# Kernel optimization log

Measured on AMD Instinct MI355X. Metric: run time of the kernel, lower is better.

Reference implementation:

```python
import jax, jax.numpy as jnp
import numpy as np

R, E, A, F, K = 1024, 512, 128, 32, 31  # rnn_dim, embed_dim, attn_dim, n_filters, kernel
B, T = 64, 2048


def setup_inputs() -> dict:
    key = jax.random.key(0)
    ks = jax.random.split(key, 10)
    return {
        "attention_hidden": jax.random.normal(ks[0], (B, R), jnp.float32),
        "memory": jax.random.normal(ks[1], (B, T, E), jnp.float32),
        "attention_weights_cat": jax.random.uniform(ks[2], (B, 2, T), jnp.float32),
        "mask": jax.random.randint(ks[3], (B, T), 0, 2, jnp.int32),
        "W_query": jax.random.normal(ks[4], (R, A), jnp.float32) / np.sqrt(R),
        "W_memory": jax.random.normal(ks[5], (E, A), jnp.float32) / np.sqrt(E),
        "conv_w": jax.random.normal(ks[6], (F, 2, K), jnp.float32) / np.sqrt(2 * K),  # OIH
        "W_loc": jax.random.normal(ks[7], (F, A), jnp.float32) / np.sqrt(F),
        "v_w": jax.random.normal(ks[8], (A,), jnp.float32) / np.sqrt(A),
        "v_b": jax.random.normal(ks[9], (1,), jnp.float32) * 0.0,
    }


def reference(attention_hidden, memory, attention_weights_cat, mask,
              W_query, W_memory, conv_w, W_loc, v_w, v_b):
    # processed query: (B, A)
    pq = attention_hidden @ W_query
    # processed memory: (B, T, A)
    pm = jnp.einsum('bte,ea->bta', memory, W_memory)
    # location features: conv1d over (B, 2, T) with 'same' padding, no bias
    loc = jax.lax.conv_general_dilated(
        attention_weights_cat, conv_w,
        window_strides=(1,), padding=[((K - 1) // 2, (K - 1) // 2)],
        dimension_numbers=('NCH', 'OIH', 'NCH'))  # (B, F, T)
    pl = jnp.einsum('bft,fa->bta', loc, W_loc)  # (B, T, A)
    # energies: v(tanh(pm + pq + pl)) -> (B, T)
    energies = jnp.tanh(pm + pq[:, None, :] + pl) @ v_w + v_b[0]
    alignments = energies + mask.astype(energies.dtype) * -1e25
    attention_weights = jax.nn.softmax(alignments, axis=-1)
    # NOTE: original code (faithfully) uses raw alignments, not softmax weights
    attention_output = jnp.einsum('bt,bte->be', alignments, memory)
    return attention_output, attention_weights
```

## Files before the change

### kernel.cpp

```cpp
#include <hip/hip_runtime.h>

#define Bsz 64
#define Tsz 2048
#define Esz 512
#define Asz 128
#define Rsz 1024
#define KP  576
#define TILE_M 32

typedef __bf16 bf16;
typedef __bf16 bf16x8 __attribute__((ext_vector_type(8)));
typedef __bf16 bf16x4 __attribute__((ext_vector_type(4)));
typedef __bf16 bf16x2 __attribute__((ext_vector_type(2)));
typedef float  f32x4  __attribute__((ext_vector_type(4)));

__global__ __launch_bounds__(256) void prep_kernel(
    const float* __restrict__ Wmem, const float* __restrict__ convw,
    const float* __restrict__ Wloc, const float* __restrict__ ah,
    const float* __restrict__ Wq, bf16* __restrict__ Wext,
    float* __restrict__ pq)
{
  __shared__ f32x4 red[256];
  int blk = blockIdx.x, tid = threadIdx.x;
  if (blk < 128) {
    int a = blk;
    #pragma unroll
    for (int e = tid; e < Esz; e += 256)
      Wext[a*KP + e] = (bf16)Wmem[e*Asz + a];
  } else if (blk < 160) {
    int idx = (blk - 128)*256 + tid;
    int a = idx >> 6, j = idx & 63;
    float u = 0.f;
    if (j < 62) {
      int c  = (j < 31) ? 0 : 1;
      int kk = (j < 31) ? j : j - 31;
      #pragma unroll
      for (int f = 0; f < 32; ++f)
        u += convw[f*62 + c*31 + kk] * Wloc[f*Asz + a];
    }
    Wext[a*KP + Esz + j] = (bf16)u;
  } else {
    int b  = blk - 160;
    int cg = tid & 31;
    int kg = tid >> 5;
    const float* ahb = ah + (size_t)b*Rsz;
    f32x4 s = (f32x4){0.f,0.f,0.f,0.f};
    int r0 = kg*128;
    for (int r = r0; r < r0 + 128; ++r) {
      float av = ahb[r];
      f32x4 wq = *(const f32x4*)&Wq[r*Asz + cg*4];
      s += av * wq;
    }
    red[tid] = s;
    __syncthreads();
    if (tid < 32) {
      f32x4 tot = red[tid];
      #pragma unroll
      for (int g = 1; g < 8; ++g) tot += red[g*32 + tid];
      *(f32x4*)&pq[b*Asz + tid*4] = tot;
    }
  }
}

__global__ __launch_bounds__(256) void attn_main(
    const float* __restrict__ memory, const float* __restrict__ awcat,
    const int* __restrict__ mask, const bf16* __restrict__ Wext,
    const float* __restrict__ pq, const float* __restrict__ vw,
    const float* __restrict__ vb, float* __restrict__ out,
    float* __restrict__ ws_align)
{
  __shared__ bf16  Afull[TILE_M * KP];
  __shared__ float s_pq[Asz];
  __shared__ float s_vw[Asz];
  __shared__ float s_ebuf[TILE_M];
  __shared__ float s_align[TILE_M];

  int tid = threadIdx.x;
  int b  = blockIdx.x >> 6;
  int t0 = (blockIdx.x & 63) << 5;

  const float4* memv = (const float4*)(memory + (size_t)(b*Tsz + t0)*Esz);
  #pragma unroll
  for (int i = tid; i < TILE_M*(Esz/4); i += 256) {
    int r = i >> 7, c4 = i & 127;
    float4 v = memv[r*128 + c4];
    int k = c4 * 4;
    int sw = (k >> 3) ^ (r & 7);
    int base = r*KP + sw*8 + (k & 7);
    bf16x4 p; p[0]=(bf16)v.x; p[1]=(bf16)v.y; p[2]=(bf16)v.z; p[3]=(bf16)v.w;
    *(bf16x4*)&Afull[base] = p;
  }
  const float* aw = awcat + (size_t)b*2*Tsz;
  #pragma unroll
  for (int i = tid; i < TILE_M*64; i += 256) {
    int r = i >> 6, j = i & 63;
    float val = 0.f;
    if (j < 62) {
      int c  = (j < 31) ? 0 : 1;
      int kk = (j < 31) ? j : j - 31;
      int t  = t0 + r + kk - 15;
      if (t >= 0 && t < Tsz) val = aw[c*Tsz + t];
    }
    int k = Esz + j;
    int sw = (k >> 3) ^ (r & 7);
    Afull[r*KP + sw*8 + (k & 7)] = (bf16)val;
  }
  if (tid < Asz) { s_pq[tid] = pq[b*Asz + tid]; s_vw[tid] = vw[tid]; }
  if (tid < TILE_M) s_ebuf[tid] = 0.f;
  __syncthreads();

  int w = tid >> 6, l = tid & 63;
  int quad = l >> 4, lrow = l & 15;

  f32x4 acc[2][2];
  #pragma unroll
  for (int mt = 0; mt < 2; ++mt)
    #pragma unroll
    for (int nt = 0; nt < 2; ++nt)
      acc[mt][nt] = (f32x4){0.f, 0.f, 0.f, 0.f};

  for (int kc = 0; kc < KP/32; ++kc) {
    int kbase = kc*32 + quad*8;
    bf16x8 bfrag[2];
    #pragma unroll
    for (int nt = 0; nt < 2; ++nt) {
      int acol = lrow + 16*(2*w + nt);
      bfrag[nt] = *(const bf16x8*)&Wext[acol*KP + kbase];
    }
    bf16x8 afrag[2];
    #pragma unroll
    for (int mt = 0; mt < 2; ++mt) {
      int r = mt*16 + lrow;
      int sw = ((kbase >> 3) ^ (r & 7));
      afrag[mt] = *(const bf16x8*)&Afull[r*KP + sw*8];
    }
    #pragma unroll
    for (int mt = 0; mt < 2; ++mt)
      #pragma unroll
      for (int nt = 0; nt < 2; ++nt)
        acc[mt][nt] = __builtin_amdgcn_mfma_f32_16x16x32_bf16(
            afrag[mt], bfrag[nt], acc[mt][nt], 0, 0, 0);
  }

  float partial[2][4];
  #pragma unroll
  for (int mt = 0; mt < 2; ++mt)
    #pragma unroll
    for (int rg = 0; rg < 4; ++rg) partial[mt][rg] = 0.f;
  #pragma unroll
  for (int nt = 0; nt < 2; ++nt) {
    int col = 16*(2*w + nt) + lrow;
    float vwc = s_vw[col], pqc = s_pq[col];
    #pragma unroll
    for (int mt = 0; mt < 2; ++mt)
      #pragma unroll
      for (int rg = 0; rg < 4; ++rg)
        partial[mt][rg] += tanhf(acc[mt][nt][rg] + pqc) * vwc;
  }
  #pragma unroll
  for (int off = 1; off < 16; off <<= 1)
    #pragma unroll
    for (int mt = 0; mt < 2; ++mt)
      #pragma unroll
      for (int rg = 0; rg < 4; ++rg)
        partial[mt][rg] += __shfl_xor(partial[mt][rg], off, 64);
  if (lrow == 0) {
    #pragma unroll
    for (int mt = 0; mt < 2; ++mt)
      #pragma unroll
      for (int rg = 0; rg < 4; ++rg)
        atomicAdd(&s_ebuf[mt*16 + quad*4 + rg], partial[mt][rg]);
  }
  __syncthreads();

  if (tid < TILE_M) {
    int t = t0 + tid;
    float al = s_ebuf[tid] + vb[0] + (float)mask[b*Tsz + t] * -1e25f;
    s_align[tid] = al;
    ws_align[b*Tsz + t] = al;
  }
  __syncthreads();

  int k0 = tid * 2;
  float a0 = 0.f, a1 = 0.f;
  #pragma unroll
  for (int r = 0; r < TILE_M; ++r) {
    float al = s_align[r];
    int sw = ((k0 >> 3) ^ (r & 7));
    bf16x2 m = *(const bf16x2*)&Afull[r*KP + sw*8 + (k0 & 7)];
    a0 += al * (float)m[0];
    a1 += al * (float)m[1];
  }
  atomicAdd(&out[b*Esz + k0],     a0);
  atomicAdd(&out[b*Esz + k0 + 1], a1);
}

__global__ __launch_bounds__(256) void softmax_kernel(
    const float* __restrict__ ws_align, float* __restrict__ out_w)
{
  int b = blockIdx.x, tid = threadIdx.x;
  const float* row = ws_align + (size_t)b*Tsz;
  float vals[8];
  float lmax = -3.4e38f;
  #pragma unroll
  for (int i = 0; i < 8; ++i) { vals[i] = row[tid + i*256]; lmax = fmaxf(lmax, vals[i]); }
  #pragma unroll
  for (int off = 1; off < 64; off <<= 1) lmax = fmaxf(lmax, __shfl_xor(lmax, off, 64));
  __shared__ float smax[4], ssum[4];
  if ((tid & 63) == 0) smax[tid >> 6] = lmax;
  __syncthreads();
  float bmax = fmaxf(fmaxf(smax[0], smax[1]), fmaxf(smax[2], smax[3]));
  float lsum = 0.f;
  #pragma unroll
  for (int i = 0; i < 8; ++i) { vals[i] = __expf(vals[i] - bmax); lsum += vals[i]; }
  #pragma unroll
  for (int off = 1; off < 64; off <<= 1) lsum += __shfl_xor(lsum, off, 64);
  if ((tid & 63) == 0) ssum[tid >> 6] = lsum;
  __syncthreads();
  float inv = 1.f / (ssum[0] + ssum[1] + ssum[2] + ssum[3]);
  #pragma unroll
  for (int i = 0; i < 8; ++i) out_w[(size_t)b*Tsz + tid + i*256] = vals[i] * inv;
}

extern "C" void kernel_launch(void* const* d_in, const int* in_sizes, int n_in,
                              void* d_out, int out_size, void* d_ws, size_t ws_size,
                              hipStream_t stream) {
  const float* ah   = (const float*)d_in[0];
  const float* mem  = (const float*)d_in[1];
  const float* awc  = (const float*)d_in[2];
  const int*   mask = (const int*)d_in[3];
  const float* Wq   = (const float*)d_in[4];
  const float* Wm   = (const float*)d_in[5];
  const float* cw   = (const float*)d_in[6];
  const float* Wl   = (const float*)d_in[7];
  const float* vw   = (const float*)d_in[8];
  const float* vb   = (const float*)d_in[9];
  float* out = (float*)d_out;

  bf16*  Wext = (bf16*)d_ws;
  float* pq   = (float*)((char*)d_ws + 147456);
  float* wsa  = (float*)((char*)d_ws + 180224);

  hipMemsetAsync(out, 0, Bsz*Esz*sizeof(float), stream);
  prep_kernel<<<dim3(224), 256, 0, stream>>>(Wm, cw, Wl, ah, Wq, Wext, pq);
  attn_main<<<dim3(Bsz*(Tsz/TILE_M)), 256, 0, stream>>>(mem, awc, mask, Wext, pq, vw, vb, out, wsa);
  softmax_kernel<<<dim3(Bsz), 256, 0, stream>>>(wsa, out + Bsz*Esz);
}
```

Baseline: 496.6 us.

## Process four T-tiles per block with register prefetch and reblocked Wext layout

Each attn_main block now handles 128 timesteps as four 32-row tiles, prefetching the next tile's memory rows into registers while the current tile's MFMA and epilogue run. The output is accumulated in registers across tiles, so global atomics drop fourfold. Wext is re-laid out in k-group-major blocks of 8 so B-fragment loads are contiguous across lanes. Launch bounds request 4 blocks per CU. The risks are higher register pressure from the 16 float4 prefetch buffer and fewer blocks (1024), which lowers parallelism on a memory-bound kernel.

After: 667.4 us. 1.34x slower.

```diff
diff --git a/kernel.cpp b/kernel.cpp
--- a/kernel.cpp
+++ b/kernel.cpp
@@ -7,12 +7,15 @@
 #define Rsz 1024
 #define KP  576
 #define TILE_M 32
+#define NTILES 4
+#define CHUNK (TILE_M*NTILES)
 
 typedef __bf16 bf16;
 typedef __bf16 bf16x8 __attribute__((ext_vector_type(8)));
 typedef __bf16 bf16x4 __attribute__((ext_vector_type(4)));
 typedef __bf16 bf16x2 __attribute__((ext_vector_type(2)));
 typedef float  f32x4  __attribute__((ext_vector_type(4)));
+
 
 __global__ __launch_bounds__(256) void prep_kernel(
     const float* __restrict__ Wmem, const float* __restrict__ convw,
@@ -26,7 +29,7 @@
     int a = blk;
     #pragma unroll
     for (int e = tid; e < Esz; e += 256)
-      Wext[a*KP + e] = (bf16)Wmem[e*Asz + a];
+      Wext[(size_t)(e >> 3)*(Asz*8) + a*8 + (e & 7)] = (bf16)Wmem[e*Asz + a];
   } else if (blk < 160) {
     int idx = (blk - 128)*256 + tid;
     int a = idx >> 6, j = idx & 63;
@@ -38,7 +41,7 @@
       for (int f = 0; f < 32; ++f)
         u += convw[f*62 + c*31 + kk] * Wloc[f*Asz + a];
     }
-    Wext[a*KP + Esz + j] = (bf16)u;
+    Wext[(size_t)(64 + (j >> 3))*(Asz*8) + a*8 + (j & 7)] = (bf16)u;
   } else {
     int b  = blk - 160;
     int cg = tid & 31;
@@ -62,7 +65,7 @@
   }
 }
 
-__global__ __launch_bounds__(256) void attn_main(
+__global__ __launch_bounds__(256, 4) void attn_main(
     const float* __restrict__ memory, const float* __restrict__ awcat,
     const int* __restrict__ mask, const bf16* __restrict__ Wext,
     const float* __restrict__ pq, const float* __restrict__ vw,
@@ -76,123 +79,143 @@
   __shared__ float s_align[TILE_M];
 
   int tid = threadIdx.x;
-  int b  = blockIdx.x >> 6;
-  int t0 = (blockIdx.x & 63) << 5;
-
-  const float4* memv = (const float4*)(memory + (size_t)(b*Tsz + t0)*Esz);
-  #pragma unroll
-  for (int i = tid; i < TILE_M*(Esz/4); i += 256) {
-    int r = i >> 7, c4 = i & 127;
-    float4 v = memv[r*128 + c4];
-    int k = c4 * 4;
-    int sw = (k >> 3) ^ (r & 7);
-    int base = r*KP + sw*8 + (k & 7);
-    bf16x4 p; p[0]=(bf16)v.x; p[1]=(bf16)v.y; p[2]=(bf16)v.z; p[3]=(bf16)v.w;
-    *(bf16x4*)&Afull[base] = p;
+  int b     = blockIdx.x >> 4;
+  int tbase = (blockIdx.x & 15) * CHUNK;
+
+  const float4* memv = (const float4*)memory + (size_t)(b*Tsz + tbase)*(Esz/4);
+  const float*  aw   = awcat + (size_t)b*2*Tsz;
+
+  if (tid < Asz) { s_pq[tid] = pq[b*Asz + tid]; s_vw[tid] = vw[tid]; }
+
+  float4 pre[16];
+  #pragma unroll
+  for (int p = 0; p < 16; ++p) {
+    int i = tid + p*256;
+    pre[p] = memv[(i >> 7)*128 + (i & 127)];
   }
-  const float* aw = awcat + (size_t)b*2*Tsz;
-  #pragma unroll
-  for (int i = tid; i < TILE_M*64; i += 256) {
-    int r = i >> 6, j = i & 63;
-    float val = 0.f;
-    if (j < 62) {
-      int c  = (j < 31) ? 0 : 1;
-      int kk = (j < 31) ? j : j - 31;
-      int t  = t0 + r + kk - 15;
-      if (t >= 0 && t < Tsz) val = aw[c*Tsz + t];
-    }
-    int k = Esz + j;
-    int sw = (k >> 3) ^ (r & 7);
-    Afull[r*KP + sw*8 + (k & 7)] = (bf16)val;
-  }
-  if (tid < Asz) { s_pq[tid] = pq[b*Asz + tid]; s_vw[tid] = vw[tid]; }
-  if (tid < TILE_M) s_ebuf[tid] = 0.f;
-  __syncthreads();
 
   int w = tid >> 6, l = tid & 63;
   int quad = l >> 4, lrow = l & 15;
-
-  f32x4 acc[2][2];
-  #pragma unroll
-  for (int mt = 0; mt < 2; ++mt)
-    #pragma unroll
-    for (int nt = 0; nt < 2; ++nt)
-      acc[mt][nt] = (f32x4){0.f, 0.f, 0.f, 0.f};
-
-  for (int kc = 0; kc < KP/32; ++kc) {
-    int kbase = kc*32 + quad*8;
-    bf16x8 bfrag[2];
+  float outa0 = 0.f, outa1 = 0.f;
+  int k0 = tid * 2;
+
+  #pragma unroll 1
+  for (int j = 0; j < NTILES; ++j) {
+    if (tid < TILE_M) s_ebuf[tid] = 0.f;
+    #pragma unroll
+    for (int p = 0; p < 16; ++p) {
+      int i = tid + p*256;
+      int r = i >> 7, c4 = i & 127;
+      int k = c4 * 4;
+      int sw = (k >> 3) ^ (r & 7);
+      bf16x4 pk; pk[0]=(bf16)pre[p].x; pk[1]=(bf16)pre[p].y; pk[2]=(bf16)pre[p].z; pk[3]=(bf16)pre[p].w;
+      *(bf16x4*)&Afull[r*KP + sw*8 + (k & 7)] = pk;
+    }
+    #pragma unroll
+    for (int i2 = tid; i2 < TILE_M*64; i2 += 256) {
+      int r = i2 >> 6, jj = i2 & 63;
+      float val = 0.f;
+      if (jj < 62) {
+        int c  = (jj < 31) ? 0 : 1;
+        int kk = (jj < 31) ? jj : jj - 31;
+        int t  = tbase + j*TILE_M + r + kk - 15;
+        if (t >= 0 && t < Tsz) val = aw[c*Tsz + t];
+      }
+      int k = Esz + jj;
+      int sw = (k >> 3) ^ (r & 7);
+      Afull[r*KP + sw*8 + (k & 7)] = (bf16)val;
+    }
+    __syncthreads();
+
+    if (j + 1 < NTILES) {
+      #pragma unroll
+      for (int p = 0; p < 16; ++p) {
+        int i = tid + p*256;
+        pre[p] = memv[(j+1)*(TILE_M*Esz/4) + (i >> 7)*128 + (i & 127)];
+      }
+    }
+
+    f32x4 acc[2][2];
+    #pragma unroll
+    for (int mt = 0; mt < 2; ++mt)
+      #pragma unroll
+      for (int nt = 0; nt < 2; ++nt)
+        acc[mt][nt] = (f32x4){0.f, 0.f, 0.f, 0.f};
+
+    for (int kc = 0; kc < KP/32; ++kc) {
+      int kg = kc*4 + quad;
+      bf16x8 bfrag[2];
+      #pragma unroll
+      for (int nt = 0; nt < 2; ++nt) {
+        int acol = lrow + 16*(2*w + nt);
+        bfrag[nt] = *(const bf16x8*)&Wext[((size_t)kg*Asz + acol)*8];
+      }
+      bf16x8 afrag[2];
+      #pragma unroll
+      for (int mt = 0; mt < 2; ++mt) {
+        int r = mt*16 + lrow;
+        afrag[mt] = *(const bf16x8*)&Afull[r*KP + ((kg ^ (r & 7)) << 3)];
+      }
+      #pragma unroll
+      for (int mt = 0; mt < 2; ++mt)
+        #pragma unroll
+        for (int nt = 0; nt < 2; ++nt)
+          acc[mt][nt] = __builtin_amdgcn_mfma_f32_16x16x32_bf16(
+              afrag[mt], bfrag[nt], acc[mt][nt], 0, 0, 0);
+    }
+
+    float partial[2][4];
+    #pragma unroll
+    for (int mt = 0; mt < 2; ++mt)
+      #pragma unroll
+      for (int rg = 0; rg < 4; ++rg) partial[mt][rg] = 0.f;
     #pragma unroll
     for (int nt = 0; nt < 2; ++nt) {
-      int acol = lrow + 16*(2*w + nt);
-      bfrag[nt] = *(const bf16x8*)&Wext[acol*KP + kbase];
-    }
-    bf16x8 afrag[2];
-    #pragma unroll
-    for (int mt = 0; mt < 2; ++mt) {
-      int r = mt*16 + lrow;
-      int sw = ((kbase >> 3) ^ (r & 7));
-      afrag[mt] = *(const bf16x8*)&Afull[r*KP + sw*8];
-    }
-    #pragma unroll
-    for (int mt = 0; mt < 2; ++mt)
-      #pragma unroll
-      for (int nt = 0; nt < 2; ++nt)
-        acc[mt][nt] = __builtin_amdgcn_mfma_f32_16x16x32_bf16(
-            afrag[mt], bfrag[nt], acc[mt][nt], 0, 0, 0);
+      int col = 16*(2*w + nt) + lrow;
+      float vwc = s_vw[col], pqc = s_pq[col];
+      #pragma unroll
+      for (int mt = 0; mt < 2; ++mt)
+        #pragma unroll
+        for (int rg = 0; rg < 4; ++rg)
+          partial[mt][rg] += tanhf(acc[mt][nt][rg] + pqc) * vwc;
+    }
+    #pragma unroll
+    for (int off = 1; off < 16; off <<= 1)
+      #pragma unroll
+      for (int mt = 0; mt < 2; ++mt)
+        #pragma unroll
+        for (int rg = 0; rg < 4; ++rg)
+          partial[mt][rg] += __shfl_xor(partial[mt][rg], off, 64);
+    if (lrow == 0) {
+      #pragma unroll
+      for (int mt = 0; mt < 2; ++mt)
+        #pragma unroll
+        for (int rg = 0; rg < 4; ++rg)
+          atomicAdd(&s_ebuf[mt*16 + quad*4 + rg], partial[mt][rg]);
+    }
+    __syncthreads();
+
+    if (tid < TILE_M) {
+      int t = tbase + j*TILE_M + tid;
+      float al = s_ebuf[tid] + vb[0] + (float)mask[b*Tsz + t] * -1e25f;
+      s_align[tid] = al;
+      ws_align[b*Tsz + t] = al;
+    }
+    __syncthreads();
+
+    #pragma unroll
+    for (int r = 0; r < TILE_M; ++r) {
+      float al = s_align[r];
+      int sw = ((k0 >> 3) ^ (r & 7));
+      bf16x2 m = *(const bf16x2*)&Afull[r*KP + sw*8 + (k0 & 7)];
+      outa0 += al * (float)m[0];
+      outa1 += al * (float)m[1];
+    }
+    __syncthreads();
   }
 
-  float partial[2][4];
-  #pragma unroll
-  for (int mt = 0; mt < 2; ++mt)
-    #pragma unroll
-    for (int rg = 0; rg < 4; ++rg) partial[mt][rg] = 0.f;
-  #pragma unroll
-  for (int nt = 0; nt < 2; ++nt) {
-    int col = 16*(2*w + nt) + lrow;
-    float vwc = s_vw[col], pqc = s_pq[col];
-    #pragma unroll
-    for (int mt = 0; mt < 2; ++mt)
-      #pragma unroll
-      for (int rg = 0; rg < 4; ++rg)
-        partial[mt][rg] += tanhf(acc[mt][nt][rg] + pqc) * vwc;
-  }
-  #pragma unroll
-  for (int off = 1; off < 16; off <<= 1)
-    #pragma unroll
-    for (int mt = 0; mt < 2; ++mt)
-      #pragma unroll
-      for (int rg = 0; rg < 4; ++rg)
-        partial[mt][rg] += __shfl_xor(partial[mt][rg], off, 64);
-  if (lrow == 0) {
-    #pragma unroll
-    for (int mt = 0; mt < 2; ++mt)
-      #pragma unroll
-      for (int rg = 0; rg < 4; ++rg)
-        atomicAdd(&s_ebuf[mt*16 + quad*4 + rg], partial[mt][rg]);
-  }
-  __syncthreads();
-
-  if (tid < TILE_M) {
-    int t = t0 + tid;
-    float al = s_ebuf[tid] + vb[0] + (float)mask[b*Tsz + t] * -1e25f;
-    s_align[tid] = al;
-    ws_align[b*Tsz + t] = al;
-  }
-  __syncthreads();
-
-  int k0 = tid * 2;
-  float a0 = 0.f, a1 = 0.f;
-  #pragma unroll
-  for (int r = 0; r < TILE_M; ++r) {
-    float al = s_align[r];
-    int sw = ((k0 >> 3) ^ (r & 7));
-    bf16x2 m = *(const bf16x2*)&Afull[r*KP + sw*8 + (k0 & 7)];
-    a0 += al * (float)m[0];
-    a1 += al * (float)m[1];
-  }
-  atomicAdd(&out[b*Esz + k0],     a0);
-  atomicAdd(&out[b*Esz + k0 + 1], a1);
+  atomicAdd(&out[b*Esz + k0],     outa0);
+  atomicAdd(&out[b*Esz + k0 + 1], outa1);
 }
 
 __global__ __launch_bounds__(256) void softmax_kernel(
@@ -243,6 +266,6 @@
 
   hipMemsetAsync(out, 0, Bsz*Esz*sizeof(float), stream);
   prep_kernel<<<dim3(224), 256, 0, stream>>>(Wm, cw, Wl, ah, Wq, Wext, pq);
-  attn_main<<<dim3(Bsz*(Tsz/TILE_M)), 256, 0, stream>>>(mem, awc, mask, Wext, pq, vw, vb, out, wsa);
+  attn_main<<<dim3(Bsz*(Tsz/CHUNK)), 256, 0, stream>>>(mem, awc, mask, Wext, pq, vw, vb, out, wsa);
   softmax_kernel<<<dim3(Bsz), 256, 0, stream>>>(wsa, out + Bsz*Esz);
 }
```

## Restructure attention main kernel to single-wave 16-row tiles with register-direct MFMA operands

Applied to the files above, without the earlier changes.

Replaces the 256-thread, 32-row block with 64-thread single-wave blocks, each computing a 16-row tile across all 128 attention columns. Memory rows are loaded from global straight into MFMA A fragments and also staged to LDS for the output reduction. Wext is re-laid out k-chunk-major so B fragments load coalesced. tanhf is replaced by an exp-based approximation. This removes the full-tile LDS staging, the shared-memory atomics and most barriers, but doubles the number of global atomics on the output and re-reads the weights from global/L2 in every block.

New measurement: 583.0 us. +17.4%, slower.

```diff
diff --git a/kernel.cpp b/kernel.cpp
--- a/kernel.cpp
+++ b/kernel.cpp
@@ -6,13 +6,13 @@
 #define Asz 128
 #define Rsz 1024
 #define KP  576
-#define TILE_M 32
+#define WROWS 16
+#define LPAD 520
 
 typedef __bf16 bf16;
 typedef __bf16 bf16x8 __attribute__((ext_vector_type(8)));
-typedef __bf16 bf16x4 __attribute__((ext_vector_type(4)));
-typedef __bf16 bf16x2 __attribute__((ext_vector_type(2)));
 typedef float  f32x4  __attribute__((ext_vector_type(4)));
+
 
 __global__ __launch_bounds__(256) void prep_kernel(
     const float* __restrict__ Wmem, const float* __restrict__ convw,
@@ -26,7 +26,7 @@
     int a = blk;
     #pragma unroll
     for (int e = tid; e < Esz; e += 256)
-      Wext[a*KP + e] = (bf16)Wmem[e*Asz + a];
+      Wext[(size_t)(e >> 3)*(Asz*8) + a*8 + (e & 7)] = (bf16)Wmem[e*Asz + a];
   } else if (blk < 160) {
     int idx = (blk - 128)*256 + tid;
     int a = idx >> 6, j = idx & 63;
@@ -38,7 +38,7 @@
       for (int f = 0; f < 32; ++f)
         u += convw[f*62 + c*31 + kk] * Wloc[f*Asz + a];
     }
-    Wext[a*KP + Esz + j] = (bf16)u;
+    Wext[(size_t)(64 + (j >> 3))*(Asz*8) + a*8 + (j & 7)] = (bf16)u;
   } else {
     int b  = blk - 160;
     int cg = tid & 31;
@@ -62,137 +62,130 @@
   }
 }
 
-__global__ __launch_bounds__(256) void attn_main(
+__device__ __forceinline__ float tanh_fast(float x) {
+  float ex = __expf(2.f * x);
+  return 1.f - 2.f / (ex + 1.f);
+}
+
+__global__ __launch_bounds__(64) void attn_main(
     const float* __restrict__ memory, const float* __restrict__ awcat,
     const int* __restrict__ mask, const bf16* __restrict__ Wext,
     const float* __restrict__ pq, const float* __restrict__ vw,
     const float* __restrict__ vb, float* __restrict__ out,
     float* __restrict__ ws_align)
 {
-  __shared__ bf16  Afull[TILE_M * KP];
-  __shared__ float s_pq[Asz];
-  __shared__ float s_vw[Asz];
-  __shared__ float s_ebuf[TILE_M];
-  __shared__ float s_align[TILE_M];
-
-  int tid = threadIdx.x;
-  int b  = blockIdx.x >> 6;
-  int t0 = (blockIdx.x & 63) << 5;
-
-  const float4* memv = (const float4*)(memory + (size_t)(b*Tsz + t0)*Esz);
-  #pragma unroll
-  for (int i = tid; i < TILE_M*(Esz/4); i += 256) {
-    int r = i >> 7, c4 = i & 127;
-    float4 v = memv[r*128 + c4];
-    int k = c4 * 4;
-    int sw = (k >> 3) ^ (r & 7);
-    int base = r*KP + sw*8 + (k & 7);
-    bf16x4 p; p[0]=(bf16)v.x; p[1]=(bf16)v.y; p[2]=(bf16)v.z; p[3]=(bf16)v.w;
-    *(bf16x4*)&Afull[base] = p;
-  }
+  __shared__ bf16 tile[WROWS * LPAD];
+
+  int l    = threadIdx.x;
+  int quad = l >> 4, lrow = l & 15;
+  int b    = blockIdx.x >> 7;
+  int t0   = (blockIdx.x & 127) << 4;
+
+  float pqv[8], vwv[8];
+  #pragma unroll
+  for (int nt = 0; nt < 8; ++nt) {
+    pqv[nt] = pq[b*Asz + 16*nt + lrow];
+    vwv[nt] = vw[16*nt + lrow];
+  }
+  int maskv[4];
+  #pragma unroll
+  for (int rg = 0; rg < 4; ++rg)
+    maskv[rg] = mask[b*Tsz + t0 + quad*4 + rg];
+  float vb0 = vb[0];
+
   const float* aw = awcat + (size_t)b*2*Tsz;
-  #pragma unroll
-  for (int i = tid; i < TILE_M*64; i += 256) {
-    int r = i >> 6, j = i & 63;
-    float val = 0.f;
-    if (j < 62) {
-      int c  = (j < 31) ? 0 : 1;
-      int kk = (j < 31) ? j : j - 31;
-      int t  = t0 + r + kk - 15;
-      if (t >= 0 && t < Tsz) val = aw[c*Tsz + t];
-    }
-    int k = Esz + j;
-    int sw = (k >> 3) ^ (r & 7);
-    Afull[r*KP + sw*8 + (k & 7)] = (bf16)val;
-  }
-  if (tid < Asz) { s_pq[tid] = pq[b*Asz + tid]; s_vw[tid] = vw[tid]; }
-  if (tid < TILE_M) s_ebuf[tid] = 0.f;
+  float awv[2][8];
+  #pragma unroll
+  for (int g = 0; g < 2; ++g)
+    #pragma unroll
+    for (int j = 0; j < 8; ++j) {
+      int jloc = g*32 + quad*8 + j;
+      float v = 0.f;
+      if (jloc < 62) {
+        int c  = (jloc < 31) ? 0 : 1;
+        int kk = (jloc < 31) ? jloc : jloc - 31;
+        int t  = t0 + lrow + kk - 15;
+        if (t >= 0 && t < Tsz) v = aw[c*Tsz + t];
+      }
+      awv[g][j] = v;
+    }
+
+  const float* ap = memory + ((size_t)(b*Tsz) + t0 + lrow)*Esz + quad*8;
+  const bf16*  bp = Wext + ((size_t)quad*Asz + lrow)*8;
+
+  f32x4 acc[8];
+  #pragma unroll
+  for (int nt = 0; nt < 8; ++nt) acc[nt] = (f32x4){0.f,0.f,0.f,0.f};
+
+  #pragma unroll
+  for (int kc = 0; kc < 16; ++kc) {
+    f32x4 aA = *(const f32x4*)(ap + kc*32);
+    f32x4 aB = *(const f32x4*)(ap + kc*32 + 4);
+    bf16x8 bfr[8];
+    #pragma unroll
+    for (int nt = 0; nt < 8; ++nt)
+      bfr[nt] = *(const bf16x8*)(bp + (size_t)kc*4096 + nt*128);
+    bf16x8 af;
+    #pragma unroll
+    for (int j = 0; j < 4; ++j) { af[j] = (bf16)aA[j]; af[4+j] = (bf16)aB[j]; }
+    *(bf16x8*)&tile[lrow*LPAD + kc*32 + quad*8] = af;
+    #pragma unroll
+    for (int nt = 0; nt < 8; ++nt)
+      acc[nt] = __builtin_amdgcn_mfma_f32_16x16x32_bf16(af, bfr[nt], acc[nt], 0, 0, 0);
+  }
+  #pragma unroll
+  for (int g = 0; g < 2; ++g) {
+    bf16x8 bfr[8];
+    #pragma unroll
+    for (int nt = 0; nt < 8; ++nt)
+      bfr[nt] = *(const bf16x8*)(bp + (size_t)(16+g)*4096 + nt*128);
+    bf16x8 af;
+    #pragma unroll
+    for (int j = 0; j < 8; ++j) af[j] = (bf16)awv[g][j];
+    #pragma unroll
+    for (int nt = 0; nt < 8; ++nt)
+      acc[nt] = __builtin_amdgcn_mfma_f32_16x16x32_bf16(af, bfr[nt], acc[nt], 0, 0, 0);
+  }
+
+  float partial[4];
+  #pragma unroll
+  for (int rg = 0; rg < 4; ++rg) partial[rg] = 0.f;
+  #pragma unroll
+  for (int nt = 0; nt < 8; ++nt)
+    #pragma unroll
+    for (int rg = 0; rg < 4; ++rg)
+      partial[rg] += tanh_fast(acc[nt][rg] + pqv[nt]) * vwv[nt];
+  #pragma unroll
+  for (int off = 1; off < 16; off <<= 1)
+    #pragma unroll
+    for (int rg = 0; rg < 4; ++rg)
+      partial[rg] += __shfl_xor(partial[rg], off, 64);
+
+  float alignv[4];
+  #pragma unroll
+  for (int rg = 0; rg < 4; ++rg)
+    alignv[rg] = partial[rg] + vb0 + (float)maskv[rg] * -1e25f;
+  if (lrow == 0) {
+    #pragma unroll
+    for (int rg = 0; rg < 4; ++rg)
+      ws_align[b*Tsz + t0 + quad*4 + rg] = alignv[rg];
+  }
+
   __syncthreads();
 
-  int w = tid >> 6, l = tid & 63;
-  int quad = l >> 4, lrow = l & 15;
-
-  f32x4 acc[2][2];
-  #pragma unroll
-  for (int mt = 0; mt < 2; ++mt)
-    #pragma unroll
-    for (int nt = 0; nt < 2; ++nt)
-      acc[mt][nt] = (f32x4){0.f, 0.f, 0.f, 0.f};
-
-  for (int kc = 0; kc < KP/32; ++kc) {
-    int kbase = kc*32 + quad*8;
-    bf16x8 bfrag[2];
-    #pragma unroll
-    for (int nt = 0; nt < 2; ++nt) {
-      int acol = lrow + 16*(2*w + nt);
-      bfrag[nt] = *(const bf16x8*)&Wext[acol*KP + kbase];
-    }
-    bf16x8 afrag[2];
-    #pragma unroll
-    for (int mt = 0; mt < 2; ++mt) {
-      int r = mt*16 + lrow;
-      int sw = ((kbase >> 3) ^ (r & 7));
-      afrag[mt] = *(const bf16x8*)&Afull[r*KP + sw*8];
-    }
-    #pragma unroll
-    for (int mt = 0; mt < 2; ++mt)
-      #pragma unroll
-      for (int nt = 0; nt < 2; ++nt)
-        acc[mt][nt] = __builtin_amdgcn_mfma_f32_16x16x32_bf16(
-            afrag[mt], bfrag[nt], acc[mt][nt], 0, 0, 0);
-  }
-
-  float partial[2][4];
-  #pragma unroll
-  for (int mt = 0; mt < 2; ++mt)
-    #pragma unroll
-    for (int rg = 0; rg < 4; ++rg) partial[mt][rg] = 0.f;
-  #pragma unroll
-  for (int nt = 0; nt < 2; ++nt) {
-    int col = 16*(2*w + nt) + lrow;
-    float vwc = s_vw[col], pqc = s_pq[col];
-    #pragma unroll
-    for (int mt = 0; mt < 2; ++mt)
-      #pragma unroll
-      for (int rg = 0; rg < 4; ++rg)
-        partial[mt][rg] += tanhf(acc[mt][nt][rg] + pqc) * vwc;
-  }
-  #pragma unroll
-  for (int off = 1; off < 16; off <<= 1)
-    #pragma unroll
-    for (int mt = 0; mt < 2; ++mt)
-      #pragma unroll
-      for (int rg = 0; rg < 4; ++rg)
-        partial[mt][rg] += __shfl_xor(partial[mt][rg], off, 64);
-  if (lrow == 0) {
-    #pragma unroll
-    for (int mt = 0; mt < 2; ++mt)
-      #pragma unroll
-      for (int rg = 0; rg < 4; ++rg)
-        atomicAdd(&s_ebuf[mt*16 + quad*4 + rg], partial[mt][rg]);
-  }
-  __syncthreads();
-
-  if (tid < TILE_M) {
-    int t = t0 + tid;
-    float al = s_ebuf[tid] + vb[0] + (float)mask[b*Tsz + t] * -1e25f;
-    s_align[tid] = al;
-    ws_align[b*Tsz + t] = al;
-  }
-  __syncthreads();
-
-  int k0 = tid * 2;
-  float a0 = 0.f, a1 = 0.f;
-  #pragma unroll
-  for (int r = 0; r < TILE_M; ++r) {
-    float al = s_align[r];
-    int sw = ((k0 >> 3) ^ (r & 7));
-    bf16x2 m = *(const bf16x2*)&Afull[r*KP + sw*8 + (k0 & 7)];
-    a0 += al * (float)m[0];
-    a1 += al * (float)m[1];
-  }
-  atomicAdd(&out[b*Esz + k0],     a0);
-  atomicAdd(&out[b*Esz + k0 + 1], a1);
+  float outv[8];
+  #pragma unroll
+  for (int j = 0; j < 8; ++j) outv[j] = 0.f;
+  #pragma unroll
+  for (int r = 0; r < WROWS; ++r) {
+    float al = __shfl(alignv[r & 3], (r >> 2) * 16, 64);
+    bf16x8 m = *(const bf16x8*)&tile[r*LPAD + l*8];
+    #pragma unroll
+    for (int j = 0; j < 8; ++j) outv[j] += al * (float)m[j];
+  }
+  float* op = out + b*Esz + l*8;
+  #pragma unroll
+  for (int j = 0; j < 8; ++j) atomicAdd(op + j, outv[j]);
 }
 
 __global__ __launch_bounds__(256) void softmax_kernel(
@@ -243,6 +236,6 @@
 
   hipMemsetAsync(out, 0, Bsz*Esz*sizeof(float), stream);
   prep_kernel<<<dim3(224), 256, 0, stream>>>(Wm, cw, Wl, ah, Wq, Wext, pq);
-  attn_main<<<dim3(Bsz*(Tsz/TILE_M)), 256, 0, stream>>>(mem, awc, mask, Wext, pq, vw, vb, out, wsa);
+  attn_main<<<dim3(Bsz*(Tsz/WROWS)), 64, 0, stream>>>(mem, awc, mask, Wext, pq, vw, vb, out, wsa);
   softmax_kernel<<<dim3(Bsz), 256, 0, stream>>>(wsa, out + Bsz*Esz);
 }
```
